# Optimization experiments

Hardware: AMD Instinct MI355X
Metric: run time of the kernel (lower is better)

Reference implementation:

```python
import jax, jax.numpy as jnp
import numpy as np

B, S, H, NH = 4, 1024, 2048, 16
HD = H // NH  # 128


def _rotate_half(x):
    x1, x2 = jnp.split(x, 2, axis=-1)
    return jnp.concatenate([-x2, x1], axis=-1)


def setup_inputs() -> dict:
    key = jax.random.key(0)
    ks = jax.random.split(key, 8)
    hidden_states = jax.random.normal(ks[0], (B, S, H), dtype=jnp.float32)
    k_in = jax.random.normal(ks[1], (B * NH, HD, S), dtype=jnp.float32)  # [B*nh, hd, K]
    v_in = jax.random.normal(ks[2], (B, NH, S, HD), dtype=jnp.float32)   # [B, nh, K, hd]
    # causal additive mask [B, 1, Q, K]
    i = jnp.arange(S)[:, None]
    j = jnp.arange(S)[None, :]
    mask = jnp.where(j <= i, 0.0, -1e9).astype(jnp.float32)
    attention_mask = jnp.broadcast_to(mask, (B, 1, S, S))
    # RoPE tables [S, hd]
    inv_freq = 1.0 / (10000.0 ** (jnp.arange(0, HD, 2, dtype=jnp.float32) / HD))
    freqs = jnp.arange(S, dtype=jnp.float32)[:, None] * inv_freq[None, :]  # [S, hd/2]
    emb = jnp.concatenate([freqs, freqs], axis=-1)  # [S, hd]
    rope_cos = jnp.cos(emb)
    rope_sin = jnp.sin(emb)
    std = 0.02
    wq = jax.random.normal(ks[3], (H, H), dtype=jnp.float32) * std
    bq = jnp.zeros((H,), dtype=jnp.float32)
    wo = jax.random.normal(ks[4], (H, H), dtype=jnp.float32) * (std / np.sqrt(2 * 24))
    bo = jnp.zeros((H,), dtype=jnp.float32)
    return {"hidden_states": hidden_states, "key": k_in, "value": v_in,
            "attention_mask": attention_mask, "rope_cos": rope_cos,
            "rope_sin": rope_sin, "wq": wq, "bq": bq, "wo": wo, "bo": bo}


def reference(hidden_states, key, value, attention_mask, rope_cos, rope_sin, wq, bq, wo, bo):
    dtype = hidden_states.dtype
    scale = 1.0 / np.sqrt(HD)
    # q projection -> [B, nh, Q, hd]
    q = hidden_states @ wq.T + bq
    q = q.reshape(B, S, NH, HD).transpose(0, 2, 1, 3)
    # RoPE on query only
    cos = rope_cos[None, None, :, :]
    sin = rope_sin[None, None, :, :]
    q = q * cos + _rotate_half(q) * sin
    # scores: key is [B*nh, hd, K]
    k = key.reshape(B, NH, HD, S)
    scores = jnp.einsum('bhqd,bhdk->bhqk', q, k) * scale + attention_mask
    probs = jax.nn.softmax(scores.astype(jnp.float32), axis=-1).astype(dtype)
    # attention output -> [B, Q, H]
    out = jnp.einsum('bhqk,bhkd->bqhd', probs, value).reshape(B, S, H)
    out = out @ wo.T + bo
    return out
```

## Files before the change

### kernel.cpp

```cpp
#include <hip/hip_runtime.h>
#include <cstdint>


typedef unsigned short u16;
typedef __bf16 bf16x8 __attribute__((ext_vector_type(8)));
typedef float  f32x4  __attribute__((ext_vector_type(4)));

__device__ __forceinline__ u16 f2bf(float f) {
  uint32_t u = __builtin_bit_cast(uint32_t, f);
  u += 0x7fffu + ((u >> 16) & 1u);
  return (u16)(u >> 16);
}
__device__ __forceinline__ float bf2f(u16 h) {
  uint32_t u = ((uint32_t)h) << 16;
  return __builtin_bit_cast(float, u);
}
__device__ __forceinline__ void gld16(const void* g, void* l) {
  __builtin_amdgcn_global_load_lds(
      (const __attribute__((address_space(1))) void*)g,
      (__attribute__((address_space(3))) void*)l, 16, 0, 0);
}

__global__ __launch_bounds__(256) void cvt_kernel(const float* __restrict__ in,
                                                  u16* __restrict__ out, int n4) {
  int i = blockIdx.x * 256 + threadIdx.x;
  if (i < n4) {
    float4 v = ((const float4*)in)[i];
    ushort4 o;
    o.x = f2bf(v.x); o.y = f2bf(v.y); o.z = f2bf(v.z); o.w = f2bf(v.w);
    ((ushort4*)out)[i] = o;
  }
}

__global__ __launch_bounds__(256) void transpose_cvt(const float* __restrict__ in,
                                                     u16* __restrict__ out, int R, int C) {
  __shared__ float tile[32][33];
  const int bh = blockIdx.x;
  const int nct = C >> 5;
  const int rt = blockIdx.y / nct, ct = blockIdx.y % nct;
  const float* src = in + (size_t)bh * R * C;
  u16* dst = out + (size_t)bh * R * C;
  const int r = threadIdx.x >> 3, c4 = (threadIdx.x & 7) * 4;
  float4 v = *(const float4*)(src + (size_t)(rt * 32 + r) * C + ct * 32 + c4);
  tile[r][c4 + 0] = v.x; tile[r][c4 + 1] = v.y;
  tile[r][c4 + 2] = v.z; tile[r][c4 + 3] = v.w;
  __syncthreads();
  ushort4 o;
  o.x = f2bf(tile[c4 + 0][r]); o.y = f2bf(tile[c4 + 1][r]);
  o.z = f2bf(tile[c4 + 2][r]); o.w = f2bf(tile[c4 + 3][r]);
  *(ushort4*)(dst + (size_t)(ct * 32 + r) * R + rt * 32 + c4) = o;
}

template<bool OUT_BF16>
__global__ __launch_bounds__(256, 2)
void gemm_bt(const u16* __restrict__ A, const u16* __restrict__ Bm,
             const float* __restrict__ bias, void* __restrict__ Cout,
             int M, int N, int K) {
  __shared__ __align__(16) u16 As[128 * 32];
  __shared__ __align__(16) u16 Bs[128 * 32];
  const int t = threadIdx.x, lane = t & 63, w = t >> 6;
  const int row0 = blockIdx.x * 128, col0 = blockIdx.y * 128;
  const int wr = (w >> 1) * 64, wc = (w & 1) * 64;
  const int fr = lane & 15, fg = lane >> 4, fk = fg * 8;
  const int srow = w * 32 + (lane >> 2), scol = (lane & 3) * 8;
  const u16* gA0 = A  + (size_t)(row0 + srow) * K + scol;
  const u16* gB0 = Bm + (size_t)(col0 + srow) * K + scol;
  u16* lA0 = As + (w * 32) * 32;
  u16* lA1 = As + (w * 32 + 16) * 32;
  u16* lB0 = Bs + (w * 32) * 32;
  u16* lB1 = Bs + (w * 32 + 16) * 32;
  f32x4 acc[4][4] = {};

  for (int k0 = 0; k0 < K; k0 += 32) {
    __syncthreads();
    gld16(gA0 + k0, lA0);
    gld16(gA0 + k0 + (size_t)16 * K, lA1);
    gld16(gB0 + k0, lB0);
    gld16(gB0 + k0 + (size_t)16 * K, lB1);
    __syncthreads();
    bf16x8 af[4], bq[4];
#pragma unroll
    for (int i = 0; i < 4; i++) af[i] = *(const bf16x8*)&As[(wr + i * 16 + fr) * 32 + fk];
#pragma unroll
    for (int i = 0; i < 4; i++) bq[i] = *(const bf16x8*)&Bs[(wc + i * 16 + fr) * 32 + fk];
#pragma unroll
    for (int mi = 0; mi < 4; mi++)
#pragma unroll
      for (int ni = 0; ni < 4; ni++)
        acc[mi][ni] = __builtin_amdgcn_mfma_f32_16x16x32_bf16(af[mi], bq[ni], acc[mi][ni], 0, 0, 0);
  }

#pragma unroll
  for (int mi = 0; mi < 4; mi++)
#pragma unroll
    for (int ni = 0; ni < 4; ni++) {
      int col = col0 + wc + ni * 16 + fr;
      float bv = bias[col];
#pragma unroll
      for (int i = 0; i < 4; i++) {
        int row = row0 + wr + mi * 16 + fg * 4 + i;
        float v = acc[mi][ni][i] + bv;
        if constexpr (OUT_BF16) ((u16*)Cout)[(size_t)row * N + col] = f2bf(v);
        else                    ((float*)Cout)[(size_t)row * N + col] = v;
      }
    }
}

__global__ __launch_bounds__(256, 2)
void gemm_rope(const u16* __restrict__ A, const u16* __restrict__ Bm,
               const float* __restrict__ bias, const float* __restrict__ cosb,
               const float* __restrict__ sinb, u16* __restrict__ qout) {
  __shared__ __align__(16) u16 As[128 * 32];
  __shared__ __align__(16) u16 Bs[128 * 32];
  const int K = 2048;
  const int t = threadIdx.x, lane = t & 63, w = t >> 6;
  const int row0 = blockIdx.x * 128, h = blockIdx.y;
  const int wr = (w >> 1) * 64, g = w & 1;
  const int fr = lane & 15, fg = lane >> 4, fk = fg * 8;
  const int srow = w * 32 + (lane >> 2), scol = (lane & 3) * 8;
  const u16* gA0 = A  + (size_t)(row0 + srow) * K + scol;
  const u16* gB0 = Bm + (size_t)(h * 128 + srow) * K + scol;
  u16* lA0 = As + (w * 32) * 32;
  u16* lA1 = As + (w * 32 + 16) * 32;
  u16* lB0 = Bs + (w * 32) * 32;
  u16* lB1 = Bs + (w * 32 + 16) * 32;
  f32x4 acc[4][4] = {};
  const int colr[4] = {g * 32 + fr, g * 32 + 16 + fr,
                       g * 32 + 64 + fr, g * 32 + 80 + fr};

  for (int k0 = 0; k0 < K; k0 += 32) {
    __syncthreads();
    gld16(gA0 + k0, lA0);
    gld16(gA0 + k0 + (size_t)16 * K, lA1);
    gld16(gB0 + k0, lB0);
    gld16(gB0 + k0 + (size_t)16 * K, lB1);
    __syncthreads();
    bf16x8 af[4], bq[4];
#pragma unroll
    for (int i = 0; i < 4; i++) af[i] = *(const bf16x8*)&As[(wr + i * 16 + fr) * 32 + fk];
#pragma unroll
    for (int ni = 0; ni < 4; ni++) bq[ni] = *(const bf16x8*)&Bs[colr[ni] * 32 + fk];
#pragma unroll
    for (int mi = 0; mi < 4; mi++)
#pragma unroll
      for (int ni = 0; ni < 4; ni++)
        acc[mi][ni] = __builtin_amdgcn_mfma_f32_16x16x32_bf16(af[mi], bq[ni], acc[mi][ni], 0, 0, 0);
  }

  float bv[4];
#pragma unroll
  for (int ni = 0; ni < 4; ni++) bv[ni] = bias[h * 128 + colr[ni]];
#pragma unroll
  for (int mi = 0; mi < 4; mi++)
#pragma unroll
    for (int i = 0; i < 4; i++) {
      int row = row0 + wr + mi * 16 + fg * 4 + i;
      int s = row & 1023, bb = row >> 10;
      size_t obase = (((size_t)(bb * 16 + h)) * 1024 + s) * 128;
#pragma unroll
      for (int dp = 0; dp < 2; dp++) {
        int d = g * 32 + dp * 16 + fr;
        float c  = cosb[s * 128 + d];
        float sn = sinb[s * 128 + d];
        float qlo = acc[mi][dp][i] + bv[dp];
        float qhi = acc[mi][dp + 2][i] + bv[dp + 2];
        qout[obase + d]      = f2bf(qlo * c - qhi * sn);
        qout[obase + d + 64] = f2bf(qhi * c + qlo * sn);
      }
    }
}

__global__ __launch_bounds__(256, 2)
void attn_kernel(const u16* __restrict__ qbf, const u16* __restrict__ kTb,
                 const u16* __restrict__ vTb, u16* __restrict__ aout) {
  __shared__ __align__(16) u16 Kb[2][64 * 128];
  __shared__ __align__(16) u16 Vb[2][128 * 64];
  __shared__ __align__(16) u16 Pb[4][16 * 72];
  const int t = threadIdx.x, lane = t & 63, w = t >> 6;
  const int x = blockIdx.x;
  const int xi = x >> 3;
  const int bh = (x & 7) * 8 + (xi & 7);
  const int jp = xi >> 3;
  const int b = bh >> 4, h = bh & 15;
  const int fr = lane & 15, fg = lane >> 4, frs = fr & 7;
  const float scale = 0.088388347648318447f;
  const u16* kbase = kTb + (size_t)bh * 131072;
  const u16* vbase = vTb + (size_t)bh * 131072;
  u16* Pw = Pb[w];

  const int kr  = t >> 4;
  const int kcs = ((t & 15) ^ (kr & 7)) * 8;
  const int vr  = t >> 3;
  const int vcs = ((t & 7) ^ (vr & 7)) * 8;

  for (int pass = 0; pass < 2; pass++) {
    const int j = pass ? 15 - jp : jp;
    const int q0 = j * 64;
    const int ntiles = j + 1;
    bf16x8 qf[4];
#pragma unroll
    for (int kb = 0; kb < 4; kb++)
      qf[kb] = *(const bf16x8*)&qbf[((size_t)bh * 1024 + q0 + w * 16 + fr) * 128 + kb * 32 + fg * 8];
    f32x4 acc[8] = {};
    float m[4], l[4];
#pragma unroll
    for (int i = 0; i < 4; i++) { m[i] = -3e38f; l[i] = 0.f; }

    auto STAGE = [&](int kt, int buf) {
      const u16* ks = kbase + (size_t)(kt * 64) * 128;
      const u16* vs = vbase + kt * 64;
#pragma unroll
      for (int p = 0; p < 4; p++)
        gld16(ks + (size_t)(p * 16 + kr) * 128 + kcs, &Kb[buf][(p * 256 + t) * 8]);
#pragma unroll
      for (int p = 0; p < 4; p++)
        gld16(vs + (size_t)(p * 32 + vr) * 1024 + vcs, &Vb[buf][(p * 256 + t) * 8]);
    };

    STAGE(0, 0);
    __syncthreads();
    int cur = 0;
    for (int kt = 0; kt < ntiles; kt++) {
      if (kt + 1 < ntiles) STAGE(kt + 1, cur ^ 1);
      f32x4 sa[4] = {};
      __builtin_amdgcn_s_setprio(1);
#pragma unroll
      for (int kb = 0; kb < 4; kb++) {
        bf16x8 kf[4];
#pragma unroll
        for (int ni = 0; ni < 4; ni++)
          kf[ni] = *(const bf16x8*)&Kb[cur][(ni * 16 + fr) * 128 + (((kb * 4 + fg) ^ frs) * 8)];
#pragma unroll
        for (int ni = 0; ni < 4; ni++)
          sa[ni] = __builtin_amdgcn_mfma_f32_16x16x32_bf16(qf[kb], kf[ni], sa[ni], 0, 0, 0);
      }
      __builtin_amdgcn_s_setprio(0);
      const bool diag = (kt == j);
      float tmax[4] = {-3e38f, -3e38f, -3e38f, -3e38f};
      if (diag) {
        const int rloc = w * 16 + fg * 4;
#pragma unroll
        for (int ni = 0; ni < 4; ni++) {
          int cloc = ni * 16 + fr;
#pragma unroll
          for (int i = 0; i < 4; i++) {
            float s = sa[ni][i] * scale;
            if (cloc > rloc + i) s = -1e9f;
            sa[ni][i] = s;
            tmax[i] = fmaxf(tmax[i], s);
          }
        }
      } else {
#pragma unroll
        for (int ni = 0; ni < 4; ni++)
#pragma unroll
          for (int i = 0; i < 4; i++) {
            float s = sa[ni][i] * scale;
            sa[ni][i] = s;
            tmax[i] = fmaxf(tmax[i], s);
          }
      }
#pragma unroll
      for (int msk = 1; msk < 16; msk <<= 1)
#pragma unroll
        for (int i = 0; i < 4; i++) tmax[i] = fmaxf(tmax[i], __shfl_xor(tmax[i], msk));
      float need = fmaxf(fmaxf(tmax[0] - m[0], tmax[1] - m[1]),
                         fmaxf(tmax[2] - m[2], tmax[3] - m[3]));
      if (!__all(need <= 8.f)) {
#pragma unroll
        for (int i = 0; i < 4; i++) {
          float mn = fmaxf(m[i], tmax[i]);
          float corr = __expf(m[i] - mn);
          m[i] = mn;
          l[i] *= corr;
#pragma unroll
          for (int ni = 0; ni < 8; ni++) acc[ni][i] *= corr;
        }
      }
      float rs[4] = {0.f, 0.f, 0.f, 0.f};
#pragma unroll
      for (int ni = 0; ni < 4; ni++)
#pragma unroll
        for (int i = 0; i < 4; i++) {
          float p = __expf(sa[ni][i] - m[i]);
          sa[ni][i] = p;
          rs[i] += p;
        }
#pragma unroll
      for (int msk = 1; msk < 16; msk <<= 1)
#pragma unroll
        for (int i = 0; i < 4; i++) rs[i] += __shfl_xor(rs[i], msk);
#pragma unroll
      for (int i = 0; i < 4; i++) l[i] += rs[i];
#pragma unroll
      for (int ni = 0; ni < 4; ni++)
#pragma unroll
        for (int i = 0; i < 4; i++)
          Pw[(fg * 4 + i) * 72 + ni * 16 + fr] = f2bf(sa[ni][i]);
      __builtin_amdgcn_s_setprio(1);
#pragma unroll
      for (int k2 = 0; k2 < 2; k2++) {
        bf16x8 pf = *(const bf16x8*)&Pw[fr * 72 + k2 * 32 + fg * 8];
#pragma unroll
        for (int ni = 0; ni < 8; ni++) {
          bf16x8 vf = *(const bf16x8*)&Vb[cur][(ni * 16 + fr) * 64 + (((k2 * 4 + fg) ^ frs) * 8)];
          acc[ni] = __builtin_amdgcn_mfma_f32_16x16x32_bf16(pf, vf, acc[ni], 0, 0, 0);
        }
      }
      __builtin_amdgcn_s_setprio(0);
      __syncthreads();
      cur ^= 1;
    }
#pragma unroll
    for (int i = 0; i < 4; i++) {
      int s = q0 + w * 16 + fg * 4 + i;
      float inv = 1.f / l[i];
#pragma unroll
      for (int ni = 0; ni < 8; ni++)
        aout[(((size_t)b * 1024 + s) * 16 + h) * 128 + ni * 16 + fr] = f2bf(acc[ni][i] * inv);
    }
    if (pass == 0) __syncthreads();
  }
}

extern "C" void kernel_launch(void* const* d_in, const int* in_sizes, int n_in,
                              void* d_out, int out_size, void* d_ws, size_t ws_size,
                              hipStream_t stream) {
  const float* hs  = (const float*)d_in[0];
  const float* key = (const float*)d_in[1];
  const float* val = (const float*)d_in[2];
  const float* rc  = (const float*)d_in[4];
  const float* rs  = (const float*)d_in[5];
  const float* wq  = (const float*)d_in[6];
  const float* bq  = (const float*)d_in[7];
  const float* wo  = (const float*)d_in[8];
  const float* bo  = (const float*)d_in[9];
  float* out = (float*)d_out;

  char* ws = (char*)d_ws;
  u16* hs_bf = (u16*)(ws);
  u16* wq_bf = (u16*)(ws + 16777216);
  u16* wo_bf = (u16*)(ws + 25165824);
  u16* q_bf  = (u16*)(ws + 33554432);
  u16* kT    = (u16*)(ws + 50331648);
  u16* vT    = (u16*)(ws + 67108864);
  u16* attn_bf = hs_bf;

  cvt_kernel<<<8192, 256, 0, stream>>>(hs, hs_bf, 8388608 / 4);
  cvt_kernel<<<4096, 256, 0, stream>>>(wq, wq_bf, 4194304 / 4);
  cvt_kernel<<<4096, 256, 0, stream>>>(wo, wo_bf, 4194304 / 4);

  transpose_cvt<<<dim3(64, 128), 256, 0, stream>>>(key, kT, 128, 1024);
  transpose_cvt<<<dim3(64, 128), 256, 0, stream>>>(val, vT, 1024, 128);

  gemm_rope<<<dim3(32, 16), 256, 0, stream>>>(hs_bf, wq_bf, bq, rc, rs, q_bf);
  attn_kernel<<<512, 256, 0, stream>>>(q_bf, kT, vT, attn_bf);
  gemm_bt<false><<<dim3(32, 16), 256, 0, stream>>>(attn_bf, wo_bf, bo, out, 4096, 2048, 2048);
}
```

Measured before the change: 180.0 us.

## Rewrite attention with 32x32 MFMA, 2 waves per block, register P

```diff
diff --git a/kernel.cpp b/kernel.cpp
--- a/kernel.cpp
+++ b/kernel.cpp
@@ -5,6 +5,8 @@
 typedef unsigned short u16;
 typedef __bf16 bf16x8 __attribute__((ext_vector_type(8)));
 typedef float  f32x4  __attribute__((ext_vector_type(4)));
+typedef float  f32x16 __attribute__((ext_vector_type(16)));
+typedef uint32_t u32x4 __attribute__((ext_vector_type(4)));
 
 __device__ __forceinline__ u16 f2bf(float f) {
   uint32_t u = __builtin_bit_cast(uint32_t, f);
@@ -14,6 +16,9 @@
 __device__ __forceinline__ float bf2f(u16 h) {
   uint32_t u = ((uint32_t)h) << 16;
   return __builtin_bit_cast(float, u);
+}
+__device__ __forceinline__ uint32_t pkbf(float a, float b) {
+  return (uint32_t)f2bf(a) | ((uint32_t)f2bf(b) << 16);
 }
 __device__ __forceinline__ void gld16(const void* g, void* l) {
   __builtin_amdgcn_global_load_lds(
@@ -170,51 +175,50 @@
     }
 }
 
-__global__ __launch_bounds__(256, 2)
+__global__ __launch_bounds__(128, 1)
 void attn_kernel(const u16* __restrict__ qbf, const u16* __restrict__ kTb,
                  const u16* __restrict__ vTb, u16* __restrict__ aout) {
   __shared__ __align__(16) u16 Kb[2][64 * 128];
   __shared__ __align__(16) u16 Vb[2][128 * 64];
-  __shared__ __align__(16) u16 Pb[4][16 * 72];
   const int t = threadIdx.x, lane = t & 63, w = t >> 6;
   const int x = blockIdx.x;
-  const int xi = x >> 3;
-  const int bh = (x & 7) * 8 + (xi & 7);
-  const int jp = xi >> 3;
+  const int bh = x & 63, jp = x >> 6;
   const int b = bh >> 4, h = bh & 15;
-  const int fr = lane & 15, fg = lane >> 4, frs = fr & 7;
+  const int q31 = lane & 31, hi = lane >> 5, kx = lane & 7;
   const float scale = 0.088388347648318447f;
   const u16* kbase = kTb + (size_t)bh * 131072;
   const u16* vbase = vTb + (size_t)bh * 131072;
-  u16* Pw = Pb[w];
-
-  const int kr  = t >> 4;
-  const int kcs = ((t & 15) ^ (kr & 7)) * 8;
-  const int vr  = t >> 3;
-  const int vcs = ((t & 7) ^ (vr & 7)) * 8;
+
+  const int kR = t >> 4;
+  const int kG = ((t & 15) ^ (kR & 7)) * 8;
+  const int vR = t >> 3;
+  const int vG = ((t & 7) ^ (vR & 7)) * 8;
 
   for (int pass = 0; pass < 2; pass++) {
     const int j = pass ? 15 - jp : jp;
     const int q0 = j * 64;
+    const int rw0 = q0 + w * 32;
+    const int rowg = rw0 + q31;
     const int ntiles = j + 1;
-    bf16x8 qf[4];
-#pragma unroll
-    for (int kb = 0; kb < 4; kb++)
-      qf[kb] = *(const bf16x8*)&qbf[((size_t)bh * 1024 + q0 + w * 16 + fr) * 128 + kb * 32 + fg * 8];
-    f32x4 acc[8] = {};
-    float m[4], l[4];
-#pragma unroll
-    for (int i = 0; i < 4; i++) { m[i] = -3e38f; l[i] = 0.f; }
+
+    bf16x8 qf[8];
+#pragma unroll
+    for (int ds = 0; ds < 8; ds++)
+      qf[ds] = *(const bf16x8*)&qbf[((size_t)bh * 1024 + rowg) * 128 + ds * 16 + hi * 8];
+
+    f32x16 acc[4] = {};
+    float m = -3e38f, l = 0.f;
 
     auto STAGE = [&](int kt, int buf) {
-      const u16* ks = kbase + (size_t)(kt * 64) * 128;
-      const u16* vs = vbase + kt * 64;
-#pragma unroll
-      for (int p = 0; p < 4; p++)
-        gld16(ks + (size_t)(p * 16 + kr) * 128 + kcs, &Kb[buf][(p * 256 + t) * 8]);
-#pragma unroll
-      for (int p = 0; p < 4; p++)
-        gld16(vs + (size_t)(p * 32 + vr) * 1024 + vcs, &Vb[buf][(p * 256 + t) * 8]);
+      const u16* ksrc = kbase + (size_t)(kt * 64 + kR) * 128 + kG;
+      const u16* vsrc = vbase + (size_t)vR * 1024 + kt * 64 + vG;
+      u16* kl = &Kb[buf][t * 8];
+      u16* vl = &Vb[buf][t * 8];
+#pragma unroll
+      for (int p = 0; p < 8; p++) {
+        gld16(ksrc + (size_t)p * 8 * 128, kl + p * 1024);
+        gld16(vsrc + (size_t)p * 16 * 1024, vl + p * 1024);
+      }
     };
 
     STAGE(0, 0);
@@ -222,104 +226,97 @@
     int cur = 0;
     for (int kt = 0; kt < ntiles; kt++) {
       if (kt + 1 < ntiles) STAGE(kt + 1, cur ^ 1);
-      f32x4 sa[4] = {};
+
+      f32x16 sa0 = {}, sa1 = {};
       __builtin_amdgcn_s_setprio(1);
 #pragma unroll
-      for (int kb = 0; kb < 4; kb++) {
-        bf16x8 kf[4];
-#pragma unroll
-        for (int ni = 0; ni < 4; ni++)
-          kf[ni] = *(const bf16x8*)&Kb[cur][(ni * 16 + fr) * 128 + (((kb * 4 + fg) ^ frs) * 8)];
-#pragma unroll
-        for (int ni = 0; ni < 4; ni++)
-          sa[ni] = __builtin_amdgcn_mfma_f32_16x16x32_bf16(qf[kb], kf[ni], sa[ni], 0, 0, 0);
+      for (int ds = 0; ds < 8; ds++) {
+        bf16x8 k0 = *(const bf16x8*)&Kb[cur][q31 * 128 + (((ds * 2 + hi) ^ kx) * 8)];
+        bf16x8 k1 = *(const bf16x8*)&Kb[cur][(q31 + 32) * 128 + (((ds * 2 + hi) ^ kx) * 8)];
+        sa0 = __builtin_amdgcn_mfma_f32_32x32x16_bf16(k0, qf[ds], sa0, 0, 0, 0);
+        sa1 = __builtin_amdgcn_mfma_f32_32x32x16_bf16(k1, qf[ds], sa1, 0, 0, 0);
       }
       __builtin_amdgcn_s_setprio(0);
-      const bool diag = (kt == j);
-      float tmax[4] = {-3e38f, -3e38f, -3e38f, -3e38f};
-      if (diag) {
-        const int rloc = w * 16 + fg * 4;
-#pragma unroll
-        for (int ni = 0; ni < 4; ni++) {
-          int cloc = ni * 16 + fr;
-#pragma unroll
-          for (int i = 0; i < 4; i++) {
-            float s = sa[ni][i] * scale;
-            if (cloc > rloc + i) s = -1e9f;
-            sa[ni][i] = s;
-            tmax[i] = fmaxf(tmax[i], s);
-          }
+
+      const bool diag = (kt * 64 + 63 > rw0);
+      float mx = -3e38f;
+#pragma unroll
+      for (int r = 0; r < 16; r++) {
+        float s0 = sa0[r] * scale;
+        float s1 = sa1[r] * scale;
+        if (diag) {
+          int cr = (r & 3) + 8 * (r >> 2) + 4 * hi;
+          if (kt * 64 + cr > rowg)      s0 = -1e9f;
+          if (kt * 64 + 32 + cr > rowg) s1 = -1e9f;
         }
-      } else {
-#pragma unroll
-        for (int ni = 0; ni < 4; ni++)
-#pragma unroll
-          for (int i = 0; i < 4; i++) {
-            float s = sa[ni][i] * scale;
-            sa[ni][i] = s;
-            tmax[i] = fmaxf(tmax[i], s);
-          }
-      }
-#pragma unroll
-      for (int msk = 1; msk < 16; msk <<= 1)
-#pragma unroll
-        for (int i = 0; i < 4; i++) tmax[i] = fmaxf(tmax[i], __shfl_xor(tmax[i], msk));
-      float need = fmaxf(fmaxf(tmax[0] - m[0], tmax[1] - m[1]),
-                         fmaxf(tmax[2] - m[2], tmax[3] - m[3]));
-      if (!__all(need <= 8.f)) {
-#pragma unroll
-        for (int i = 0; i < 4; i++) {
-          float mn = fmaxf(m[i], tmax[i]);
-          float corr = __expf(m[i] - mn);
-          m[i] = mn;
-          l[i] *= corr;
-#pragma unroll
-          for (int ni = 0; ni < 8; ni++) acc[ni][i] *= corr;
+        sa0[r] = s0; sa1[r] = s1;
+        mx = fmaxf(mx, fmaxf(s0, s1));
+      }
+      mx = fmaxf(mx, __shfl_xor(mx, 32));
+      if (!__all(mx - m <= 8.f)) {
+        float mn = fmaxf(m, mx);
+        float corr = __expf(m - mn);
+        m = mn; l *= corr;
+#pragma unroll
+        for (int nd = 0; nd < 4; nd++)
+#pragma unroll
+          for (int r = 0; r < 16; r++) acc[nd][r] *= corr;
+      }
+      float sum = 0.f;
+#pragma unroll
+      for (int r = 0; r < 16; r++) {
+        float p0 = __expf(sa0[r] - m); sa0[r] = p0;
+        float p1 = __expf(sa1[r] - m); sa1[r] = p1;
+        sum += p0 + p1;
+      }
+      sum += __shfl_xor(sum, 32);
+      l += sum;
+
+      __builtin_amdgcn_s_setprio(1);
+#pragma unroll
+      for (int ks = 0; ks < 4; ks++) {
+        const int r0 = (ks & 1) * 8;
+        float p0 = (ks < 2) ? sa0[r0 + 0] : sa1[r0 + 0];
+        float p1 = (ks < 2) ? sa0[r0 + 1] : sa1[r0 + 1];
+        float p2 = (ks < 2) ? sa0[r0 + 2] : sa1[r0 + 2];
+        float p3 = (ks < 2) ? sa0[r0 + 3] : sa1[r0 + 3];
+        float p4 = (ks < 2) ? sa0[r0 + 4] : sa1[r0 + 4];
+        float p5 = (ks < 2) ? sa0[r0 + 5] : sa1[r0 + 5];
+        float p6 = (ks < 2) ? sa0[r0 + 6] : sa1[r0 + 6];
+        float p7 = (ks < 2) ? sa0[r0 + 7] : sa1[r0 + 7];
+        uint32_t w0 = pkbf(p0, p1), w1 = pkbf(p2, p3);
+        uint32_t w2 = pkbf(p4, p5), w3 = pkbf(p6, p7);
+        uint32_t x0 = __shfl_xor(w0, 32), x1 = __shfl_xor(w1, 32);
+        uint32_t x2 = __shfl_xor(w2, 32), x3 = __shfl_xor(w3, 32);
+        u32x4 aw;
+        aw.x = hi ? x2 : w0;
+        aw.y = hi ? x3 : w1;
+        aw.z = hi ? w2 : x0;
+        aw.w = hi ? w3 : x1;
+        bf16x8 af = __builtin_bit_cast(bf16x8, aw);
+#pragma unroll
+        for (int nd = 0; nd < 4; nd++) {
+          bf16x8 vf = *(const bf16x8*)&Vb[cur][(nd * 32 + q31) * 64 + (((ks * 2 + hi) ^ kx) * 8)];
+          acc[nd] = __builtin_amdgcn_mfma_f32_32x32x16_bf16(af, vf, acc[nd], 0, 0, 0);
         }
       }
-      float rs[4] = {0.f, 0.f, 0.f, 0.f};
-#pragma unroll
-      for (int ni = 0; ni < 4; ni++)
-#pragma unroll
-        for (int i = 0; i < 4; i++) {
-          float p = __expf(sa[ni][i] - m[i]);
-          sa[ni][i] = p;
-          rs[i] += p;
-        }
-#pragma unroll
-      for (int msk = 1; msk < 16; msk <<= 1)
-#pragma unroll
-        for (int i = 0; i < 4; i++) rs[i] += __shfl_xor(rs[i], msk);
-#pragma unroll
-      for (int i = 0; i < 4; i++) l[i] += rs[i];
-#pragma unroll
-      for (int ni = 0; ni < 4; ni++)
-#pragma unroll
-        for (int i = 0; i < 4; i++)
-          Pw[(fg * 4 + i) * 72 + ni * 16 + fr] = f2bf(sa[ni][i]);
-      __builtin_amdgcn_s_setprio(1);
-#pragma unroll
-      for (int k2 = 0; k2 < 2; k2++) {
-        bf16x8 pf = *(const bf16x8*)&Pw[fr * 72 + k2 * 32 + fg * 8];
-#pragma unroll
-        for (int ni = 0; ni < 8; ni++) {
-          bf16x8 vf = *(const bf16x8*)&Vb[cur][(ni * 16 + fr) * 64 + (((k2 * 4 + fg) ^ frs) * 8)];
-          acc[ni] = __builtin_amdgcn_mfma_f32_16x16x32_bf16(pf, vf, acc[ni], 0, 0, 0);
-        }
-      }
       __builtin_amdgcn_s_setprio(0);
+
       __syncthreads();
       cur ^= 1;
     }
-#pragma unroll
-    for (int i = 0; i < 4; i++) {
-      int s = q0 + w * 16 + fg * 4 + i;
-      float inv = 1.f / l[i];
-#pragma unroll
-      for (int ni = 0; ni < 8; ni++)
-        aout[(((size_t)b * 1024 + s) * 16 + h) * 128 + ni * 16 + fr] = f2bf(acc[ni][i] * inv);
+
+    float linv = 1.f / l;
+#pragma unroll
+    for (int r = 0; r < 16; r++) {
+      int cr = (r & 3) + 8 * (r >> 2) + 4 * hi;
+      float li = __shfl(linv, cr);
+      int sg = q0 + w * 32 + cr;
+      size_t obase = (((size_t)b * 1024 + sg) * 16 + h) * 128 + q31;
+#pragma unroll
+      for (int nd = 0; nd < 4; nd++)
+        aout[obase + nd * 32] = f2bf(acc[nd][r] * li);
     }
-    if (pass == 0) __syncthreads();
   }
 }
 
@@ -354,6 +351,6 @@
   transpose_cvt<<<dim3(64, 128), 256, 0, stream>>>(val, vT, 1024, 128);
 
   gemm_rope<<<dim3(32, 16), 256, 0, stream>>>(hs_bf, wq_bf, bq, rc, rs, q_bf);
-  attn_kernel<<<512, 256, 0, stream>>>(q_bf, kT, vT, attn_bf);
+  attn_kernel<<<512, 128, 0, stream>>>(q_bf, kT, vT, attn_bf);
   gemm_bt<false><<<dim3(32, 16), 256, 0, stream>>>(attn_bf, wo_bf, bo, out, 4096, 2048, 2048);
 }
```

Measured after the change: 187.1 us. 3.9% more time.
